# Optimization experiments

Measured on AMD Instinct MI355X. Metric: run time of the kernel, lower is better.

## Reference

```python
import jax, jax.numpy as jnp
import numpy as np

B, N, C, M, OUT = 4, 256, 32, 4, 64


def _uniform(k, shape, fan_in):
    s = 1.0 / np.sqrt(fan_in)
    return jax.random.uniform(k, shape, jnp.float32, -s, s)


def setup_inputs() -> dict:
    key = jax.random.key(0)
    ks = jax.random.split(key, 11)
    return {
        "x": jax.random.normal(ks[0], (B, N, N, C), jnp.float32),
        # Neighborhood / SnConv2to1 linears (in=C, out=M neighborhood channels)
        "w1_nb": _uniform(ks[1], (3 * C, M), 3 * C),
        "b1_nb": _uniform(ks[2], (M,), 3 * C),
        "w0_nb": _uniform(ks[3], (2 * C, M), 2 * C),
        "b0_nb": _uniform(ks[4], (M,), 2 * C),
        # SnConv2 linears (in channels = M*C after neighborhood product)
        "w2d": _uniform(ks[5], (2 * M * C, OUT), 2 * M * C),
        "b2d": _uniform(ks[6], (OUT,), 2 * M * C),
        "w1d": _uniform(ks[7], (3 * M * C, OUT), 3 * M * C),
        "b1d": _uniform(ks[8], (OUT,), 3 * M * C),
        "w0d": _uniform(ks[9], (2 * M * C, OUT), 2 * M * C),
        "b0d": _uniform(ks[10], (OUT,), 2 * M * C),
    }


def _contractions(x):
    # x: [B, n, n, c]; mask=None, reduction='mean' path of _get_contractions
    n = x.shape[1]
    rowsum = x.sum(axis=1) / n                      # [B, n, c]
    colsum = x.sum(axis=2) / n                      # [B, n, c]
    diag = jnp.diagonal(x, axis1=1, axis2=2)        # [B, c, n]
    rowcolsum = x.sum(axis=(1, 2)) / (n * n)        # [B, c]
    diag_sum = diag.sum(axis=-1) / n                # [B, c]  (/= sqrt(n^2))
    diag = jnp.moveaxis(diag, -1, 1)                # move_from_end -> [B, n, c]
    return rowsum, colsum, diag, rowcolsum, diag_sum


def reference(x, w1_nb, b1_nb, w0_nb, b0_nb, w2d, b2d, w1d, b1d, w0d, b0d):
    # ---- Neighborhood: SnConv2to1 -> sigmoid ----
    rs, cs, dg, rcs, ds = _contractions(x)
    obj1 = jnp.concatenate([rs, cs, dg], axis=-1)             # [B, n, 3C]
    obj0 = jnp.concatenate([rcs, ds], axis=-1)                # [B, 2C]
    node = obj1 @ w1_nb + b1_nb + (obj0 @ w0_nb + b0_nb)[:, None, :]
    neighbs = jax.nn.sigmoid(node)                            # [B, n, M]
    # ---- _neighbor_elementwise_product ----
    expanded = neighbs[:, None, :, :] * neighbs[:, :, None, :]  # [B, n, n, M]
    # channel_product: outer product over channel dims, collapsed to M*C
    xl = (expanded[..., :, None] * x[..., None, :]).reshape(B, N, N, M * C)
    # ---- SnConv2 on the localized tensor ----
    rs2, cs2, dg2, rcs2, ds2 = _contractions(xl)
    obj2d = jnp.concatenate([xl, jnp.swapaxes(xl, 1, 2)], axis=-1)  # [B,n,n,2MC]
    obj1d = jnp.concatenate([rs2, cs2, dg2], axis=-1)               # [B,n,3MC]
    obj0d = jnp.concatenate([rcs2, ds2], axis=-1)                   # [B,2MC]
    out = (obj2d @ w2d + b2d
           + (obj1d @ w1d + b1d)[:, None, :, :]
           + (obj0d @ w0d + b0d)[:, None, None, :])                 # [B,n,n,OUT]
    return out
```

## Files before the change

kernel.cpp:

```cpp
#include <hip/hip_runtime.h>
#include <math.h>

#define Bv 4
#define Nv 256
#define Cv 32
#define Mv 4
#define OUTv 64
#define MCv (Mv*Cv)

typedef _Float16 h8 __attribute__((ext_vector_type(8)));
typedef _Float16 h4 __attribute__((ext_vector_type(4)));
typedef float f4 __attribute__((ext_vector_type(4)));

__device__ __align__(16) float g_rs  [Bv * Nv * Cv];
__device__ __align__(16) float g_cs  [Bv * Nv * Cv];
__device__ __align__(16) float g_dgx [Bv * Nv * Cv];
__device__ __align__(16) float g_nb  [Bv * Nv * Mv];
__device__ __align__(16) float g_S1  [Bv * Nv * MCv];
__device__ __align__(16) float g_S2  [Bv * Nv * MCv];
__device__ __align__(16) float g_rcs2R[8 * Bv * MCv];
__device__ __align__(16) float g_ds2 [Bv * MCv];
__device__ __align__(16) float g_addv[Bv * Nv * OUTv];
__device__ __align__(16) _Float16 g_wfrag[8 * 4 * 64 * 8];

__global__ __launch_bounds__(256) void k_contract1(const float* __restrict__ x,
                                                   const float* __restrict__ w2d) {
    int bx = blockIdx.x, b = blockIdx.y;
    int t = threadIdx.x;
    if (bx >= 2 * Nv) {
        if (b != 0) return;
        int r = bx - 2 * Nv;
        if (r == 8) {
            float4 z = {0.f,0.f,0.f,0.f};
            #pragma unroll
            for (int k = 0; k < 4; k++) ((float4*)g_rcs2R)[k * 256 + t] = z;
            return;
        }
        int fi = r * 256 + t;
        int s = fi >> 8, q = (fi >> 6) & 3, lane = fi & 63;
        int k0 = s * 32 + ((lane >> 4) << 3);
        int o = q * 16 + (lane & 15);
        #pragma unroll
        for (int jj = 0; jj < 8; jj++)
            g_wfrag[fi * 8 + jj] = (_Float16)w2d[(size_t)(k0 + jj) * OUTv + o];
        return;
    }
    int c4 = t & 7, sub = t >> 3;
    const float4* xb4 = (const float4*)(x + (size_t)b * Nv * Nv * Cv);
    __shared__ float red[32][36];
    float4 acc = {0.f,0.f,0.f,0.f};
    if (bx < Nv) {
        int n = bx;
        for (int i = sub; i < Nv; i += 32) {
            float4 v = xb4[((size_t)i * Nv + n) * 8 + c4];
            acc.x += v.x; acc.y += v.y; acc.z += v.z; acc.w += v.w;
        }
        red[sub][c4*4+0] = acc.x; red[sub][c4*4+1] = acc.y;
        red[sub][c4*4+2] = acc.z; red[sub][c4*4+3] = acc.w;
        __syncthreads();
        if (t < 32) {
            float s = 0.f;
            #pragma unroll
            for (int k = 0; k < 32; k++) s += red[k][t];
            g_rs[(b * Nv + n) * Cv + t] = s * (1.0f / Nv);
        }
        if (t < 8) ((float4*)g_dgx)[(b * Nv + n) * 8 + t] = xb4[((size_t)n * Nv + n) * 8 + t];
    } else {
        int n = bx - Nv;
        for (int j = sub; j < Nv; j += 32) {
            float4 v = xb4[((size_t)n * Nv + j) * 8 + c4];
            acc.x += v.x; acc.y += v.y; acc.z += v.z; acc.w += v.w;
        }
        red[sub][c4*4+0] = acc.x; red[sub][c4*4+1] = acc.y;
        red[sub][c4*4+2] = acc.z; red[sub][c4*4+3] = acc.w;
        __syncthreads();
        if (t < 32) {
            float s = 0.f;
            #pragma unroll
            for (int k = 0; k < 32; k++) s += red[k][t];
            g_cs[(b * Nv + n) * Cv + t] = s * (1.0f / Nv);
        }
    }
}

__global__ void k_neighb(const float* __restrict__ w1, const float* __restrict__ b1,
                         const float* __restrict__ w0, const float* __restrict__ b0) {
    int b = blockIdx.x, t = threadIdx.x;
    int c = t & 31, sub = t >> 5;
    float ar = 0.f, ad = 0.f;
    for (int n = sub; n < Nv; n += 8) {
        ar += g_rs[(b * Nv + n) * Cv + c];
        ad += g_dgx[(b * Nv + n) * Cv + c];
    }
    __shared__ float red[8][64];
    __shared__ float obj0[64];
    __shared__ float t0nb[4];
    __shared__ float nbs[Nv][4];
    __shared__ float dsred[2][128];
    red[sub][c] = ar;
    red[sub][32 + c] = ad;
    __syncthreads();
    if (t < 64) {
        float s = 0.f;
        #pragma unroll
        for (int k = 0; k < 8; k++) s += red[k][t];
        obj0[t] = s * (1.0f / Nv);
    }
    __syncthreads();
    if (t < 4) {
        float v = b0[t];
        for (int k = 0; k < 2 * Cv; k++) v += obj0[k] * w0[k * Mv + t];
        t0nb[t] = v;
    }
    __syncthreads();
    int n = t;
    float node[4];
    #pragma unroll
    for (int m = 0; m < 4; m++) node[m] = t0nb[m] + b1[m];
    for (int cc = 0; cc < Cv; cc++) {
        float r = g_rs[(b * Nv + n) * Cv + cc];
        float s = g_cs[(b * Nv + n) * Cv + cc];
        float d = g_dgx[(b * Nv + n) * Cv + cc];
        #pragma unroll
        for (int m = 0; m < 4; m++)
            node[m] += r * w1[cc * Mv + m] + s * w1[(Cv + cc) * Mv + m] + d * w1[(2 * Cv + cc) * Mv + m];
    }
    #pragma unroll
    for (int m = 0; m < 4; m++) {
        float sg = 1.0f / (1.0f + expf(-node[m]));
        nbs[t][m] = sg;
        g_nb[(b * Nv + n) * Mv + m] = sg;
    }
    __syncthreads();
    {
        int mc = t & 127, h = t >> 7;
        int m = mc >> 5, cc = mc & 31;
        float s = 0.f;
        for (int k = 0; k < 128; k++) {
            int nn = h * 128 + k;
            float nv = nbs[nn][m];
            s += nv * nv * g_dgx[(b * Nv + nn) * Cv + cc];
        }
        dsred[h][mc] = s;
    }
    __syncthreads();
    if (t < 128) g_ds2[b * MCv + t] = dsred[0][t] + dsred[1][t];
}

__global__ __launch_bounds__(256) void k_wsum(const float* __restrict__ x) {
    int bx = blockIdx.x, b = blockIdx.y;
    int t = threadIdx.x, c4 = t & 7, sub = t >> 3;
    __shared__ __align__(16) float4 nbl[Nv];
    if (t < Nv) nbl[t] = ((const float4*)(g_nb + (size_t)b * Nv * Mv))[t];
    __syncthreads();
    const float4* xb4 = (const float4*)(x + (size_t)b * Nv * Nv * Cv);
    float4 a[4];
    #pragma unroll
    for (int m = 0; m < 4; m++) a[m] = {0.f,0.f,0.f,0.f};
    __shared__ float red[32][132];
    if (bx < Nv) {
        int n = bx;
        for (int i = sub; i < Nv; i += 32) {
            float4 v = xb4[((size_t)i * Nv + n) * 8 + c4];
            float4 nv = nbl[i];
            a[0].x += nv.x*v.x; a[0].y += nv.x*v.y; a[0].z += nv.x*v.z; a[0].w += nv.x*v.w;
            a[1].x += nv.y*v.x; a[1].y += nv.y*v.y; a[1].z += nv.y*v.z; a[1].w += nv.y*v.w;
            a[2].x += nv.z*v.x; a[2].y += nv.z*v.y; a[2].z += nv.z*v.z; a[2].w += nv.z*v.w;
            a[3].x += nv.w*v.x; a[3].y += nv.w*v.y; a[3].z += nv.w*v.z; a[3].w += nv.w*v.w;
        }
        #pragma unroll
        for (int m = 0; m < 4; m++) {
            red[sub][m*32 + c4*4+0] = a[m].x; red[sub][m*32 + c4*4+1] = a[m].y;
            red[sub][m*32 + c4*4+2] = a[m].z; red[sub][m*32 + c4*4+3] = a[m].w;
        }
        __syncthreads();
        if (t < 128) {
            float s = 0.f;
            #pragma unroll
            for (int k = 0; k < 32; k++) s += red[k][t];
            g_S1[(size_t)(b * Nv + n) * MCv + t] = s;
            int m = t >> 5;
            float nv = ((const float*)&nbl[n])[m];
            atomicAdd(&g_rcs2R[(((n & 7) * Bv) + b) * MCv + t], nv * s);
        }
    } else {
        int n = bx - Nv;
        for (int j = sub; j < Nv; j += 32) {
            float4 v = xb4[((size_t)n * Nv + j) * 8 + c4];
            float4 nv = nbl[j];
            a[0].x += nv.x*v.x; a[0].y += nv.x*v.y; a[0].z += nv.x*v.z; a[0].w += nv.x*v.w;
            a[1].x += nv.y*v.x; a[1].y += nv.y*v.y; a[1].z += nv.y*v.z; a[1].w += nv.y*v.w;
            a[2].x += nv.z*v.x; a[2].y += nv.z*v.y; a[2].z += nv.z*v.z; a[2].w += nv.z*v.w;
            a[3].x += nv.w*v.x; a[3].y += nv.w*v.y; a[3].z += nv.w*v.z; a[3].w += nv.w*v.w;
        }
        #pragma unroll
        for (int m = 0; m < 4; m++) {
            red[sub][m*32 + c4*4+0] = a[m].x; red[sub][m*32 + c4*4+1] = a[m].y;
            red[sub][m*32 + c4*4+2] = a[m].z; red[sub][m*32 + c4*4+3] = a[m].w;
        }
        __syncthreads();
        if (t < 128) {
            float s = 0.f;
            #pragma unroll
            for (int k = 0; k < 32; k++) s += red[k][t];
            g_S2[(size_t)(b * Nv + n) * MCv + t] = s;
        }
    }
}

__global__ __launch_bounds__(256) void k_add(const float* __restrict__ w1d,
                                             const float* __restrict__ b1d,
                                             const float* __restrict__ b2d,
                                             const float* __restrict__ w0d,
                                             const float* __restrict__ b0d) {
    int b = blockIdx.y, n0 = blockIdx.x * 2;
    int t = threadIdx.x, o = t & 63, ks = t >> 6;
    __shared__ float rcl[MCv], dsl[MCv];
    __shared__ float red0[4][64];
    __shared__ float red2[4][2][64];
    if (t < 128) {
        float s = 0.f;
        #pragma unroll
        for (int r = 0; r < 8; r++) s += g_rcs2R[(r * Bv + b) * MCv + t];
        rcl[t] = s;
    } else {
        dsl[t - 128] = g_ds2[b * MCv + (t - 128)];
    }
    __syncthreads();
    const float invN = 1.0f / Nv;
    const float invN2 = invN * invN;
    float nv0 = g_nb[(b * Nv + n0) * Mv + ks];
    float nv1 = g_nb[(b * Nv + n0 + 1) * Mv + ks];
    float f0 = nv0 * invN, d20 = nv0 * nv0;
    float f1 = nv1 * invN, d21 = nv1 * nv1;
    const float* S1a = g_S1 + (size_t)(b * Nv + n0) * MCv + ks * 32;
    const float* S1b = S1a + MCv;
    const float* S2a = g_S2 + (size_t)(b * Nv + n0) * MCv + ks * 32;
    const float* S2b = S2a + MCv;
    const float* dga = g_dgx + (size_t)(b * Nv + n0) * Cv;
    const float* dgb = dga + Cv;
    float acc0v = 0.f, accA = 0.f, accB = 0.f;
    #pragma unroll 8
    for (int cc = 0; cc < 32; cc++) {
        int mc = ks * 32 + cc;
        float w1a = w1d[(size_t)mc * OUTv + o];
        float w1b = w1d[(size_t)(MCv + mc) * OUTv + o];
        float w1c = w1d[(size_t)(2 * MCv + mc) * OUTv + o];
        float w0a = w0d[(size_t)mc * OUTv + o];
        float w0b = w0d[(size_t)(MCv + mc) * OUTv + o];
        acc0v += invN2 * rcl[mc] * w0a + invN * dsl[mc] * w0b;
        accA  += f0 * S1a[cc] * w1a + f0 * S2a[cc] * w1b + d20 * dga[cc] * w1c;
        accB  += f1 * S1b[cc] * w1a + f1 * S2b[cc] * w1b + d21 * dgb[cc] * w1c;
    }
    red0[ks][o] = acc0v;
    red2[ks][0][o] = accA;
    red2[ks][1][o] = accB;
    __syncthreads();
    if (t < 128) {
        int nn = t >> 6, oo = t & 63;
        float t0v = red0[0][oo] + red0[1][oo] + red0[2][oo] + red0[3][oo]
                  + b1d[oo] + b2d[oo] + b0d[oo];
        float v = red2[0][nn][oo] + red2[1][nn][oo] + red2[2][nn][oo] + red2[3][nn][oo] + t0v;
        g_addv[(size_t)(b * Nv + n0 + nn) * OUTv + oo] = v;
    }
}

#define XPAD 40
__global__ __launch_bounds__(256) void k_main(const float* __restrict__ x,
                                              float* __restrict__ out) {
    int jt = blockIdx.x, i = blockIdx.y, b = blockIdx.z;
    int j0 = jt * 128;
    int t = threadIdx.x;
    int lane = t & 63, w = t >> 6;
    int rowA = lane & 15, quad = lane >> 4;

    __shared__ __align__(16) _Float16 Wl[8 * 4 * 64 * 8];
    __shared__ __align__(16) _Float16 Xt[128 * XPAD];
    __shared__ __align__(16) _Float16 Xb[128 * XPAD];

    {
        const float4* src = (const float4*)g_wfrag;
        float4* dst = (float4*)Wl;
        #pragma unroll
        for (int r = 0; r < 8; r++) dst[r * 256 + t] = src[r * 256 + t];
    }
    {
        const float4* x4 = (const float4*)x;
        #pragma unroll
        for (int r = 0; r < 4; r++) {
            int idx = r * 256 + t;
            int j = idx >> 3, c4 = idx & 7;
            float4 v = x4[((size_t)(b * Nv + i) * Nv + j0 + j) * 8 + c4];
            h4 hv; hv[0] = (_Float16)v.x; hv[1] = (_Float16)v.y;
            hv[2] = (_Float16)v.z; hv[3] = (_Float16)v.w;
            *(h4*)&Xt[j * XPAD + c4 * 4] = hv;
            float4 u = x4[((size_t)(b * Nv + j0 + j) * Nv + i) * 8 + c4];
            h4 hu; hu[0] = (_Float16)u.x; hu[1] = (_Float16)u.y;
            hu[2] = (_Float16)u.z; hu[3] = (_Float16)u.w;
            *(h4*)&Xb[j * XPAD + c4 * 4] = hu;
        }
    }
    int jl1 = w * 32 + rowA, jl2 = jl1 + 16;
    _Float16 e1h[4], e2h[4];
    {
        const float* ni = g_nb + (size_t)(b * Nv + i) * Mv;
        const float* n1 = g_nb + (size_t)(b * Nv + j0 + jl1) * Mv;
        const float* n2 = g_nb + (size_t)(b * Nv + j0 + jl2) * Mv;
        #pragma unroll
        for (int m = 0; m < 4; m++) {
            e1h[m] = (_Float16)(ni[m] * n1[m]);
            e2h[m] = (_Float16)(ni[m] * n2[m]);
        }
    }
    __syncthreads();

    f4 acc[2][4];
    #pragma unroll
    for (int js = 0; js < 2; js++)
        #pragma unroll
        for (int q = 0; q < 4; q++) acc[js][q] = {0.f, 0.f, 0.f, 0.f};

    const h8* Wf = (const h8*)Wl;
    #pragma unroll
    for (int part = 0; part < 2; part++) {
        const _Float16* X = part ? Xb : Xt;
        h8 xv1 = *(const h8*)&X[jl1 * XPAD + quad * 8];
        h8 xv2 = *(const h8*)&X[jl2 * XPAD + quad * 8];
        #pragma unroll
        for (int m = 0; m < 4; m++) {
            h8 a1 = xv1 * e1h[m];
            h8 a2 = xv2 * e2h[m];
            int s = part * 4 + m;
            #pragma unroll
            for (int q = 0; q < 4; q++) {
                h8 bf = Wf[(s * 4 + q) * 64 + lane];
                acc[0][q] = __builtin_amdgcn_mfma_f32_16x16x32_f16(a1, bf, acc[0][q], 0, 0, 0);
                acc[1][q] = __builtin_amdgcn_mfma_f32_16x16x32_f16(a2, bf, acc[1][q], 0, 0, 0);
            }
        }
    }
    #pragma unroll
    for (int js = 0; js < 2; js++) {
        int jbase = j0 + w * 32 + js * 16 + quad * 4;
        #pragma unroll
        for (int q = 0; q < 4; q++) {
            int o = q * 16 + rowA;
            #pragma unroll
            for (int r = 0; r < 4; r++) {
                int j = jbase + r;
                float v = acc[js][q][r] + g_addv[(size_t)(b * Nv + j) * OUTv + o];
                out[(((size_t)(b * Nv + i)) * Nv + j) * OUTv + o] = v;
            }
        }
    }
}

extern "C" void kernel_launch(void* const* d_in, const int* in_sizes, int n_in,
                              void* d_out, int out_size, void* d_ws, size_t ws_size,
                              hipStream_t stream) {
    const float* x     = (const float*)d_in[0];
    const float* w1_nb = (const float*)d_in[1];
    const float* b1_nb = (const float*)d_in[2];
    const float* w0_nb = (const float*)d_in[3];
    const float* b0_nb = (const float*)d_in[4];
    const float* w2d   = (const float*)d_in[5];
    const float* b2d   = (const float*)d_in[6];
    const float* w1d   = (const float*)d_in[7];
    const float* b1d   = (const float*)d_in[8];
    const float* w0d   = (const float*)d_in[9];
    const float* b0d   = (const float*)d_in[10];
    float* out = (float*)d_out;
    (void)d_ws; (void)ws_size;

    hipLaunchKernelGGL(k_contract1, dim3(2 * Nv + 9, Bv), dim3(256), 0, stream, x, w2d);
    hipLaunchKernelGGL(k_neighb, dim3(Bv), dim3(256), 0, stream,
                       w1_nb, b1_nb, w0_nb, b0_nb);
    hipLaunchKernelGGL(k_wsum, dim3(2 * Nv, Bv), dim3(256), 0, stream, x);
    hipLaunchKernelGGL(k_add, dim3(Nv / 2, Bv), dim3(256), 0, stream,
                       w1d, b1d, b2d, w0d, b0d);
    hipLaunchKernelGGL(k_main, dim3(2, Nv, Bv), dim3(256), 0, stream, x, out);
}
```

Baseline: 173.6 us.

## Process two rows per main block and move diag-sum into wsum atomics

The main MFMA kernel now handles two i rows per block. This halves the grid and reuses the staged weight fragments and the g_addv loads across both rows, at the cost of twice the LDS for the X tiles and more accumulator registers. Separately, the ds2 diagonal reduction is taken out of the 4-block neighborhood kernel and done with replicated atomics inside k_wsum, then reduced in k_add. This shortens the serial low-occupancy neighb kernel.

```diff
diff --git a/kernel.cpp b/kernel.cpp
--- a/kernel.cpp
+++ b/kernel.cpp
@@ -19,7 +19,7 @@
 __device__ __align__(16) float g_S1  [Bv * Nv * MCv];
 __device__ __align__(16) float g_S2  [Bv * Nv * MCv];
 __device__ __align__(16) float g_rcs2R[8 * Bv * MCv];
-__device__ __align__(16) float g_ds2 [Bv * MCv];
+__device__ __align__(16) float g_ds2R [8 * Bv * MCv];
 __device__ __align__(16) float g_addv[Bv * Nv * OUTv];
 __device__ __align__(16) _Float16 g_wfrag[8 * 4 * 64 * 8];
 
@@ -33,7 +33,10 @@
         if (r == 8) {
             float4 z = {0.f,0.f,0.f,0.f};
             #pragma unroll
-            for (int k = 0; k < 4; k++) ((float4*)g_rcs2R)[k * 256 + t] = z;
+            for (int k = 0; k < 4; k++) {
+                ((float4*)g_rcs2R)[k * 256 + t] = z;
+                ((float4*)g_ds2R )[k * 256 + t] = z;
+            }
             return;
         }
         int fi = r * 256 + t;
@@ -95,8 +98,6 @@
     __shared__ float red[8][64];
     __shared__ float obj0[64];
     __shared__ float t0nb[4];
-    __shared__ float nbs[Nv][4];
-    __shared__ float dsred[2][128];
     red[sub][c] = ar;
     red[sub][32 + c] = ad;
     __syncthreads();
@@ -126,25 +127,8 @@
             node[m] += r * w1[cc * Mv + m] + s * w1[(Cv + cc) * Mv + m] + d * w1[(2 * Cv + cc) * Mv + m];
     }
     #pragma unroll
-    for (int m = 0; m < 4; m++) {
-        float sg = 1.0f / (1.0f + expf(-node[m]));
-        nbs[t][m] = sg;
-        g_nb[(b * Nv + n) * Mv + m] = sg;
-    }
-    __syncthreads();
-    {
-        int mc = t & 127, h = t >> 7;
-        int m = mc >> 5, cc = mc & 31;
-        float s = 0.f;
-        for (int k = 0; k < 128; k++) {
-            int nn = h * 128 + k;
-            float nv = nbs[nn][m];
-            s += nv * nv * g_dgx[(b * Nv + nn) * Cv + cc];
-        }
-        dsred[h][mc] = s;
-    }
-    __syncthreads();
-    if (t < 128) g_ds2[b * MCv + t] = dsred[0][t] + dsred[1][t];
+    for (int m = 0; m < 4; m++)
+        g_nb[(b * Nv + n) * Mv + m] = 1.0f / (1.0f + expf(-node[m]));
 }
 
 __global__ __launch_bounds__(256) void k_wsum(const float* __restrict__ x) {
@@ -179,9 +163,11 @@
             #pragma unroll
             for (int k = 0; k < 32; k++) s += red[k][t];
             g_S1[(size_t)(b * Nv + n) * MCv + t] = s;
-            int m = t >> 5;
+            int m = t >> 5, c = t & 31;
             float nv = ((const float*)&nbl[n])[m];
-            atomicAdd(&g_rcs2R[(((n & 7) * Bv) + b) * MCv + t], nv * s);
+            int rep = ((n & 7) * Bv + b) * MCv + t;
+            atomicAdd(&g_rcs2R[rep], nv * s);
+            atomicAdd(&g_ds2R [rep], nv * nv * g_dgx[(b * Nv + n) * Cv + c]);
         }
     } else {
         int n = bx - Nv;
@@ -224,7 +210,11 @@
         for (int r = 0; r < 8; r++) s += g_rcs2R[(r * Bv + b) * MCv + t];
         rcl[t] = s;
     } else {
-        dsl[t - 128] = g_ds2[b * MCv + (t - 128)];
+        int tt = t - 128;
+        float s = 0.f;
+        #pragma unroll
+        for (int r = 0; r < 8; r++) s += g_ds2R[(r * Bv + b) * MCv + tt];
+        dsl[tt] = s;
     }
     __syncthreads();
     const float invN = 1.0f / Nv;
@@ -268,15 +258,18 @@
 #define XPAD 40
 __global__ __launch_bounds__(256) void k_main(const float* __restrict__ x,
                                               float* __restrict__ out) {
-    int jt = blockIdx.x, i = blockIdx.y, b = blockIdx.z;
+    int jt = blockIdx.x, ip = blockIdx.y, b = blockIdx.z;
+    int i0 = ip * 2, i1 = i0 + 1;
     int j0 = jt * 128;
     int t = threadIdx.x;
     int lane = t & 63, w = t >> 6;
     int rowA = lane & 15, quad = lane >> 4;
 
     __shared__ __align__(16) _Float16 Wl[8 * 4 * 64 * 8];
-    __shared__ __align__(16) _Float16 Xt[128 * XPAD];
-    __shared__ __align__(16) _Float16 Xb[128 * XPAD];
+    __shared__ __align__(16) _Float16 Xt0[128 * XPAD];
+    __shared__ __align__(16) _Float16 Xb0[128 * XPAD];
+    __shared__ __align__(16) _Float16 Xt1[128 * XPAD];
+    __shared__ __align__(16) _Float16 Xb1[128 * XPAD];
 
     {
         const float4* src = (const float4*)g_wfrag;
@@ -290,52 +283,72 @@
         for (int r = 0; r < 4; r++) {
             int idx = r * 256 + t;
             int j = idx >> 3, c4 = idx & 7;
-            float4 v = x4[((size_t)(b * Nv + i) * Nv + j0 + j) * 8 + c4];
-            h4 hv; hv[0] = (_Float16)v.x; hv[1] = (_Float16)v.y;
-            hv[2] = (_Float16)v.z; hv[3] = (_Float16)v.w;
-            *(h4*)&Xt[j * XPAD + c4 * 4] = hv;
-            float4 u = x4[((size_t)(b * Nv + j0 + j) * Nv + i) * 8 + c4];
-            h4 hu; hu[0] = (_Float16)u.x; hu[1] = (_Float16)u.y;
-            hu[2] = (_Float16)u.z; hu[3] = (_Float16)u.w;
-            *(h4*)&Xb[j * XPAD + c4 * 4] = hu;
+            float4 v0 = x4[((size_t)(b * Nv + i0) * Nv + j0 + j) * 8 + c4];
+            float4 v1 = x4[((size_t)(b * Nv + i1) * Nv + j0 + j) * 8 + c4];
+            float4 u0 = x4[((size_t)(b * Nv + j0 + j) * Nv + i0) * 8 + c4];
+            float4 u1 = x4[((size_t)(b * Nv + j0 + j) * Nv + i1) * 8 + c4];
+            h4 h0; h0[0] = (_Float16)v0.x; h0[1] = (_Float16)v0.y;
+            h0[2] = (_Float16)v0.z; h0[3] = (_Float16)v0.w;
+            *(h4*)&Xt0[j * XPAD + c4 * 4] = h0;
+            h4 h1; h1[0] = (_Float16)v1.x; h1[1] = (_Float16)v1.y;
+            h1[2] = (_Float16)v1.z; h1[3] = (_Float16)v1.w;
+            *(h4*)&Xt1[j * XPAD + c4 * 4] = h1;
+            h4 g0; g0[0] = (_Float16)u0.x; g0[1] = (_Float16)u0.y;
+            g0[2] = (_Float16)u0.z; g0[3] = (_Float16)u0.w;
+            *(h4*)&Xb0[j * XPAD + c4 * 4] = g0;
+            h4 g1; g1[0] = (_Float16)u1.x; g1[1] = (_Float16)u1.y;
+            g1[2] = (_Float16)u1.z; g1[3] = (_Float16)u1.w;
+            *(h4*)&Xb1[j * XPAD + c4 * 4] = g1;
         }
     }
     int jl1 = w * 32 + rowA, jl2 = jl1 + 16;
-    _Float16 e1h[4], e2h[4];
+    _Float16 e1h0[4], e2h0[4], e1h1[4], e2h1[4];
     {
-        const float* ni = g_nb + (size_t)(b * Nv + i) * Mv;
+        const float* ni0 = g_nb + (size_t)(b * Nv + i0) * Mv;
+        const float* ni1 = g_nb + (size_t)(b * Nv + i1) * Mv;
         const float* n1 = g_nb + (size_t)(b * Nv + j0 + jl1) * Mv;
         const float* n2 = g_nb + (size_t)(b * Nv + j0 + jl2) * Mv;
         #pragma unroll
         for (int m = 0; m < 4; m++) {
-            e1h[m] = (_Float16)(ni[m] * n1[m]);
-            e2h[m] = (_Float16)(ni[m] * n2[m]);
-        }
-    }
-    __syncthreads();
-
-    f4 acc[2][4];
-    #pragma unroll
-    for (int js = 0; js < 2; js++)
-        #pragma unroll
-        for (int q = 0; q < 4; q++) acc[js][q] = {0.f, 0.f, 0.f, 0.f};
+            e1h0[m] = (_Float16)(ni0[m] * n1[m]);
+            e2h0[m] = (_Float16)(ni0[m] * n2[m]);
+            e1h1[m] = (_Float16)(ni1[m] * n1[m]);
+            e2h1[m] = (_Float16)(ni1[m] * n2[m]);
+        }
+    }
+    __syncthreads();
+
+    f4 acc[2][2][4];
+    #pragma unroll
+    for (int ii = 0; ii < 2; ii++)
+        #pragma unroll
+        for (int js = 0; js < 2; js++)
+            #pragma unroll
+            for (int q = 0; q < 4; q++) acc[ii][js][q] = {0.f, 0.f, 0.f, 0.f};
 
     const h8* Wf = (const h8*)Wl;
     #pragma unroll
     for (int part = 0; part < 2; part++) {
-        const _Float16* X = part ? Xb : Xt;
-        h8 xv1 = *(const h8*)&X[jl1 * XPAD + quad * 8];
-        h8 xv2 = *(const h8*)&X[jl2 * XPAD + quad * 8];
+        const _Float16* X0 = part ? Xb0 : Xt0;
+        const _Float16* X1 = part ? Xb1 : Xt1;
+        h8 xv1_0 = *(const h8*)&X0[jl1 * XPAD + quad * 8];
+        h8 xv2_0 = *(const h8*)&X0[jl2 * XPAD + quad * 8];
+        h8 xv1_1 = *(const h8*)&X1[jl1 * XPAD + quad * 8];
+        h8 xv2_1 = *(const h8*)&X1[jl2 * XPAD + quad * 8];
         #pragma unroll
         for (int m = 0; m < 4; m++) {
-            h8 a1 = xv1 * e1h[m];
-            h8 a2 = xv2 * e2h[m];
+            h8 a1_0 = xv1_0 * e1h0[m];
+            h8 a2_0 = xv2_0 * e2h0[m];
+            h8 a1_1 = xv1_1 * e1h1[m];
+            h8 a2_1 = xv2_1 * e2h1[m];
             int s = part * 4 + m;
             #pragma unroll
             for (int q = 0; q < 4; q++) {
                 h8 bf = Wf[(s * 4 + q) * 64 + lane];
-                acc[0][q] = __builtin_amdgcn_mfma_f32_16x16x32_f16(a1, bf, acc[0][q], 0, 0, 0);
-                acc[1][q] = __builtin_amdgcn_mfma_f32_16x16x32_f16(a2, bf, acc[1][q], 0, 0, 0);
+                acc[0][0][q] = __builtin_amdgcn_mfma_f32_16x16x32_f16(a1_0, bf, acc[0][0][q], 0, 0, 0);
+                acc[0][1][q] = __builtin_amdgcn_mfma_f32_16x16x32_f16(a2_0, bf, acc[0][1][q], 0, 0, 0);
+                acc[1][0][q] = __builtin_amdgcn_mfma_f32_16x16x32_f16(a1_1, bf, acc[1][0][q], 0, 0, 0);
+                acc[1][1][q] = __builtin_amdgcn_mfma_f32_16x16x32_f16(a2_1, bf, acc[1][1][q], 0, 0, 0);
             }
         }
     }
@@ -348,8 +361,9 @@
             #pragma unroll
             for (int r = 0; r < 4; r++) {
                 int j = jbase + r;
-                float v = acc[js][q][r] + g_addv[(size_t)(b * Nv + j) * OUTv + o];
-                out[(((size_t)(b * Nv + i)) * Nv + j) * OUTv + o] = v;
+                float av = g_addv[(size_t)(b * Nv + j) * OUTv + o];
+                out[(((size_t)(b * Nv + i0)) * Nv + j) * OUTv + o] = acc[0][js][q][r] + av;
+                out[(((size_t)(b * Nv + i1)) * Nv + j) * OUTv + o] = acc[1][js][q][r] + av;
             }
         }
     }
@@ -378,5 +392,5 @@
     hipLaunchKernelGGL(k_wsum, dim3(2 * Nv, Bv), dim3(256), 0, stream, x);
     hipLaunchKernelGGL(k_add, dim3(Nv / 2, Bv), dim3(256), 0, stream,
                        w1d, b1d, b2d, w0d, b0d);
-    hipLaunchKernelGGL(k_main, dim3(2, Nv, Bv), dim3(256), 0, stream, x, out);
-}
+    hipLaunchKernelGGL(k_main, dim3(2, Nv / 2, Bv), dim3(256), 0, stream, x, out);
+}
```

Result: faster. 169.4 us (-2.4%).
